# Kernel tuning notes

Measured on AMD Instinct MI355X. Metric: run time of the kernel, lower is better.

The kernel has to match this reference:

```python
import jax, jax.numpy as jnp
from jax import lax
import numpy as np

T, B, I, H, O = 512, 128, 256, 512, 256


def setup_inputs() -> dict:
    key = jax.random.key(0)
    ks = jax.random.split(key, 11)
    s = 0.05
    return {
        "x": jax.random.normal(ks[0], (T, B, I), dtype=jnp.float32),
        "W_ih0": jax.random.normal(ks[1], (H, I), dtype=jnp.float32) * s,
        "b_ih0": jax.random.normal(ks[2], (H,), dtype=jnp.float32) * s,
        "W_hh0": jax.random.normal(ks[3], (H, H), dtype=jnp.float32) * s,
        "b_hh0": jax.random.normal(ks[4], (H,), dtype=jnp.float32) * s,
        "W_ih1": jax.random.normal(ks[5], (H, H), dtype=jnp.float32) * s,
        "b_ih1": jax.random.normal(ks[6], (H,), dtype=jnp.float32) * s,
        "W_hh1": jax.random.normal(ks[7], (H, H), dtype=jnp.float32) * s,
        "b_hh1": jax.random.normal(ks[8], (H,), dtype=jnp.float32) * s,
        "W_fc": jax.random.normal(ks[9], (O, H), dtype=jnp.float32) * s,
        "b_fc": jax.random.normal(ks[10], (O,), dtype=jnp.float32) * s,
    }


def reference(x, W_ih0, b_ih0, W_hh0, b_hh0, W_ih1, b_ih1, W_hh1, b_hh1, W_fc, b_fc):
    # x: [T, B, I] (batch_first=False). 2-layer tanh RNN via lax.scan over time.
    Tn, Bn, _ = x.shape
    Hn = W_hh0.shape[0]
    h0 = jnp.zeros((2, Bn, Hn), dtype=x.dtype)

    def step(h, xt):
        h1 = jnp.tanh(xt @ W_ih0.T + b_ih0 + h[0] @ W_hh0.T + b_hh0)  # [B, H]
        h2 = jnp.tanh(h1 @ W_ih1.T + b_ih1 + h[1] @ W_hh1.T + b_hh1)  # [B, H]
        return jnp.stack([h1, h2]), h2

    h_final, out = lax.scan(step, h0, x)  # out: [T, B, H]
    # Faithful to source: output[:, -1, :] indexes the LAST BATCH element (batch_first=False),
    # giving [T, H]; pred is [T, O].
    pred = out[:, -1, :] @ W_fc.T + b_fc
    return pred, h_final
```

## Files before the change

kernel.cpp:

```cpp
#include <hip/hip_runtime.h>
#include <hip/hip_bf16.h>

#define TT 512
#define BB 128
#define II 256
#define HH 512
#define OO 256

#define NGB 8
#define NGN 16
#define RB  16
#define NS  32

#define PRED_SZ (TT*OO)

typedef __attribute__((ext_vector_type(8))) short bf16x8;
typedef __attribute__((ext_vector_type(4))) float f32x4;

#define WS_CNT  0
#define WS_H1   16512
#define WS_H2   (WS_H1 + 2*BB*HH*2)
#define WS_SAVE (WS_H2 + 2*BB*HH*2)
#define WS_ZERO WS_SAVE

__device__ __forceinline__ ushort f2bf(float f) {
  union { float f; unsigned u; } v; v.f = f;
  unsigned u = v.u;
  return (ushort)((u + 0x7FFFu + ((u >> 16) & 1u)) >> 16);
}

__global__ __launch_bounds__(256) void rnn_scan_kernel(
    const float* __restrict__ x,
    const float* __restrict__ Wih0, const float* __restrict__ bih0,
    const float* __restrict__ Whh0, const float* __restrict__ bhh0,
    const float* __restrict__ Wih1, const float* __restrict__ bih1,
    const float* __restrict__ Whh1, const float* __restrict__ bhh1,
    float* __restrict__ out, char* __restrict__ ws)
{
  __shared__ ushort ldsW[112*64*8];
  __shared__ float bias0[NS];
  __shared__ float bias1[NS];

  int*    cnt    = (int*)(ws + WS_CNT);
  ushort* h1buf  = (ushort*)(ws + WS_H1);
  ushort* h2buf  = (ushort*)(ws + WS_H2);
  float*  h2save = (float*)(ws + WS_SAVE);

  const int tid = threadIdx.x;
  const int gb  = blockIdx.x & 7;
  const int gn  = blockIdx.x >> 3;
  const int n0  = gn * NS;

  {
    const int lane = tid & 63;
    const int q    = tid >> 6;
    #pragma unroll 1
    for (int u = 0; u < 112; ++u) {
      const float* Wsrc; int Km; int ul;
      if (u < 16)      { Wsrc = Wih0; Km = II; ul = u; }
      else if (u < 48) { Wsrc = Whh0; Km = HH; ul = u - 16; }
      else if (u < 80) { Wsrc = Wih1; Km = HH; ul = u - 48; }
      else             { Wsrc = Whh1; Km = HH; ul = u - 80; }
      const int nk  = Km >> 5;
      const int ttl = ul / nk;
      const int kk  = ul - ttl*nk;
      const int n   = n0 + ttl*16 + (lane & 15);
      const int k   = kk*32 + (lane >> 4)*8 + q*2;
      const float2 wv = *(const float2*)(Wsrc + (size_t)n*Km + k);
      ushort2 b2; b2.x = f2bf(wv.x); b2.y = f2bf(wv.y);
      *(ushort2*)&ldsW[(u*64 + lane)*8 + q*2] = b2;
    }
    if (tid < NS) {
      bias0[tid] = bih0[n0+tid] + bhh0[n0+tid];
      bias1[tid] = bih1[n0+tid] + bhh1[n0+tid];
    }
  }
  __syncthreads();

  const int w     = tid >> 6;
  const int lane  = tid & 63;
  const int ttile = w & 1;
  const int layer = w >> 1;
  const int kq    = lane >> 4;
  const int rowg  = gb*RB + (lane & 15);
  const int c     = lane & 15;

  for (int p = 0; p <= TT; ++p) {
    f32x4 xf[16];
    if (layer == 0 && p < TT) {
      const float* xp = x + ((size_t)p*BB + rowg)*II + kq*8;
      #pragma unroll
      for (int kk = 0; kk < 8; ++kk) {
        xf[2*kk]   = *(const f32x4*)(xp + kk*32);
        xf[2*kk+1] = *(const f32x4*)(xp + kk*32 + 4);
      }
    }
    if (p > 0) {
      if (tid == 0) {
        while (__hip_atomic_load(&cnt[(p-1)*NGB + gb], __ATOMIC_ACQUIRE,
                                 __HIP_MEMORY_SCOPE_AGENT) < NGN) {
          __builtin_amdgcn_s_sleep(1);
        }
      }
      __syncthreads();
    }

    if (layer == 0) {
      if (p < TT) {
        bf16x8 af[16];
        const ushort* ap = h1buf + ((size_t)((p-1)&1)*BB + rowg)*HH + kq*8;
        #pragma unroll
        for (int kk = 0; kk < 16; ++kk) af[kk] = *(const bf16x8*)(ap + kk*32);
        f32x4 acc = {0.f,0.f,0.f,0.f};
        #pragma unroll
        for (int kk = 0; kk < 8; ++kk) {
          bf16x8 a;
          #pragma unroll
          for (int j = 0; j < 4; ++j) {
            a[j]   = (short)f2bf(xf[2*kk][j]);
            a[j+4] = (short)f2bf(xf[2*kk+1][j]);
          }
          const bf16x8 b = *(const bf16x8*)&ldsW[((0 + ttile*8 + kk)*64 + lane)*8];
          acc = __builtin_amdgcn_mfma_f32_16x16x32_bf16(a, b, acc, 0, 0, 0);
        }
        #pragma unroll
        for (int kk = 0; kk < 16; ++kk) {
          const bf16x8 b = *(const bf16x8*)&ldsW[((16 + ttile*16 + kk)*64 + lane)*8];
          acc = __builtin_amdgcn_mfma_f32_16x16x32_bf16(af[kk], b, acc, 0, 0, 0);
        }
        const float bv = bias0[ttile*16 + c];
        ushort* dst = h1buf + (size_t)(p&1)*BB*HH;
        const int col = n0 + ttile*16 + c;
        #pragma unroll
        for (int j = 0; j < 4; ++j) {
          const int r = gb*16 + kq*4 + j;
          const float v = tanhf(acc[j] + bv);
          dst[(size_t)r*HH + col] = f2bf(v);
          if (p == TT-1) out[PRED_SZ + (size_t)r*HH + col] = v;
        }
      }
    } else {
      if (p >= 1) {
        bf16x8 af[16], a2[16];
        const ushort* ap  = h1buf + ((size_t)((p-1)&1)*BB + rowg)*HH + kq*8;
        const ushort* a2p = h2buf + ((size_t)(p&1)*BB + rowg)*HH + kq*8;
        #pragma unroll
        for (int kk = 0; kk < 16; ++kk) {
          af[kk] = *(const bf16x8*)(ap  + kk*32);
          a2[kk] = *(const bf16x8*)(a2p + kk*32);
        }
        f32x4 acc = {0.f,0.f,0.f,0.f};
        #pragma unroll
        for (int kk = 0; kk < 16; ++kk) {
          const bf16x8 b = *(const bf16x8*)&ldsW[((48 + ttile*16 + kk)*64 + lane)*8];
          acc = __builtin_amdgcn_mfma_f32_16x16x32_bf16(af[kk], b, acc, 0, 0, 0);
        }
        #pragma unroll
        for (int kk = 0; kk < 16; ++kk) {
          const bf16x8 b = *(const bf16x8*)&ldsW[((80 + ttile*16 + kk)*64 + lane)*8];
          acc = __builtin_amdgcn_mfma_f32_16x16x32_bf16(a2[kk], b, acc, 0, 0, 0);
        }
        const float bv = bias1[ttile*16 + c];
        ushort* dst = h2buf + (size_t)((p-1)&1)*BB*HH;
        const int col = n0 + ttile*16 + c;
        #pragma unroll
        for (int j = 0; j < 4; ++j) {
          const int r = gb*16 + kq*4 + j;
          const float v = tanhf(acc[j] + bv);
          dst[(size_t)r*HH + col] = f2bf(v);
          if (r == BB-1) h2save[(size_t)(p-1)*HH + col] = v;
          if (p == TT) out[PRED_SZ + BB*HH + (size_t)r*HH + col] = v;
        }
      }
    }

    __syncthreads();
    if (tid == 0) {
      __hip_atomic_fetch_add(&cnt[p*NGB + gb], 1, __ATOMIC_RELEASE,
                             __HIP_MEMORY_SCOPE_AGENT);
    }
  }
}

__global__ __launch_bounds__(256) void rnn_pred_kernel(
    const float* __restrict__ Wfc, const float* __restrict__ bfc,
    const float* __restrict__ h2save, float* __restrict__ out)
{
  __shared__ float hs[HH];
  const int t = blockIdx.x;
  for (int i = threadIdx.x; i < HH; i += 256) hs[i] = h2save[(size_t)t*HH + i];
  __syncthreads();
  const int o = threadIdx.x;
  const f32x4* wr = (const f32x4*)(Wfc + (size_t)o*HH);
  f32x4 s = {0.f,0.f,0.f,0.f};
  #pragma unroll 8
  for (int k = 0; k < HH/4; ++k) {
    const f32x4 wv = wr[k];
    const f32x4 hv = *(const f32x4*)&hs[4*k];
    s += wv * hv;
  }
  out[(size_t)t*OO + o] = bfc[o] + s[0] + s[1] + s[2] + s[3];
}

extern "C" void kernel_launch(void* const* d_in, const int* in_sizes, int n_in,
                              void* d_out, int out_size, void* d_ws, size_t ws_size,
                              hipStream_t stream) {
  const float* x    = (const float*)d_in[0];
  const float* Wih0 = (const float*)d_in[1];
  const float* bih0 = (const float*)d_in[2];
  const float* Whh0 = (const float*)d_in[3];
  const float* bhh0 = (const float*)d_in[4];
  const float* Wih1 = (const float*)d_in[5];
  const float* bih1 = (const float*)d_in[6];
  const float* Whh1 = (const float*)d_in[7];
  const float* bhh1 = (const float*)d_in[8];
  const float* Wfc  = (const float*)d_in[9];
  const float* bfc  = (const float*)d_in[10];
  float* out = (float*)d_out;
  char*  ws  = (char*)d_ws;

  hipMemsetAsync(ws, 0, WS_ZERO, stream);

  rnn_scan_kernel<<<NGB*NGN, 256, 0, stream>>>(x, Wih0, bih0, Whh0, bhh0,
                                               Wih1, bih1, Whh1, bhh1, out, ws);
  rnn_pred_kernel<<<TT, 256, 0, stream>>>(Wfc, bfc, (const float*)(ws + WS_SAVE), out);
}
```

Baseline: 3.695 ms.

## Decouple RNN layers into per-wave pipelines with monotonic counters and coherent loads

Replaces the per-timestep block-wide barrier and per-step counter array with two monotonic per-batch-group counters, one per layer. Layer-0 and layer-1 waves now run independent loops and spin on the counters themselves, and layer 0 may run up to three steps ahead using a 4-deep h1 ring buffer. Cross-block h exchange uses cache-bypassing sc0 sc1 loads and stores with relaxed atomics instead of acquire/release. tanhf is replaced by an exp2/rcp approximation. Correctness now depends on the hand-written memory ordering through inline asm waitcnt, and the tanh is slightly less accurate.

```diff
diff --git a/kernel.cpp b/kernel.cpp
--- a/kernel.cpp
+++ b/kernel.cpp
@@ -16,10 +16,12 @@
 
 typedef __attribute__((ext_vector_type(8))) short bf16x8;
 typedef __attribute__((ext_vector_type(4))) float f32x4;
-
-#define WS_CNT  0
-#define WS_H1   16512
-#define WS_H2   (WS_H1 + 2*BB*HH*2)
+typedef __attribute__((ext_vector_type(4))) int   i32x4;
+
+#define WS_G1   0
+#define WS_G2   128
+#define WS_H1   256
+#define WS_H2   (WS_H1 + 4*BB*HH*2)
 #define WS_SAVE (WS_H2 + 2*BB*HH*2)
 #define WS_ZERO WS_SAVE
 
@@ -29,7 +31,32 @@
   return (ushort)((u + 0x7FFFu + ((u >> 16) & 1u)) >> 16);
 }
 
-__global__ __launch_bounds__(256) void rnn_scan_kernel(
+__device__ __forceinline__ float fast_tanh(float x) {
+  float cx = fminf(fmaxf(x, -30.f), 30.f);
+  float t  = __builtin_amdgcn_exp2f(cx * 2.885390081777927f);
+  return (t - 1.f) * __builtin_amdgcn_rcpf(t + 1.f);
+}
+
+__device__ __forceinline__ i32x4 ld_coh16B(const ushort* p) {
+  i32x4 r;
+  asm volatile("global_load_dwordx4 %0, %1, off sc0 sc1"
+               : "=v"(r) : "v"(p) : "memory");
+  return r;
+}
+__device__ __forceinline__ void st_coh2B(ushort* p, ushort v) {
+  unsigned vv = v;
+  asm volatile("global_store_short %0, %1, off sc0 sc1"
+               :: "v"(p), "v"(vv) : "memory");
+}
+
+__device__ __forceinline__ int g_load(int* a) {
+  return __hip_atomic_load(a, __ATOMIC_RELAXED, __HIP_MEMORY_SCOPE_AGENT);
+}
+__device__ __forceinline__ void g_post(int* a) {
+  __hip_atomic_fetch_add(a, 1, __ATOMIC_RELAXED, __HIP_MEMORY_SCOPE_AGENT);
+}
+
+__global__ __launch_bounds__(256, 1) void rnn_scan_kernel(
     const float* __restrict__ x,
     const float* __restrict__ Wih0, const float* __restrict__ bih0,
     const float* __restrict__ Whh0, const float* __restrict__ bhh0,
@@ -41,7 +68,8 @@
   __shared__ float bias0[NS];
   __shared__ float bias1[NS];
 
-  int*    cnt    = (int*)(ws + WS_CNT);
+  int*    g1     = (int*)(ws + WS_G1);
+  int*    g2     = (int*)(ws + WS_G2);
   ushort* h1buf  = (ushort*)(ws + WS_H1);
   ushort* h2buf  = (ushort*)(ws + WS_H2);
   float*  h2save = (float*)(ws + WS_SAVE);
@@ -85,99 +113,106 @@
   const int rowg  = gb*RB + (lane & 15);
   const int c     = lane & 15;
 
-  for (int p = 0; p <= TT; ++p) {
-    f32x4 xf[16];
-    if (layer == 0 && p < TT) {
-      const float* xp = x + ((size_t)p*BB + rowg)*II + kq*8;
-      #pragma unroll
-      for (int kk = 0; kk < 8; ++kk) {
-        xf[2*kk]   = *(const f32x4*)(xp + kk*32);
-        xf[2*kk+1] = *(const f32x4*)(xp + kk*32 + 4);
-      }
-    }
-    if (p > 0) {
-      if (tid == 0) {
-        while (__hip_atomic_load(&cnt[(p-1)*NGB + gb], __ATOMIC_ACQUIRE,
-                                 __HIP_MEMORY_SCOPE_AGENT) < NGN) {
-          __builtin_amdgcn_s_sleep(1);
+  int s1 = 0, s2 = 0;
+
+  if (layer == 0) {
+    for (int p = 0; p < TT; ++p) {
+      bf16x8 ax[8];
+      {
+        const float* xp = x + ((size_t)p*BB + rowg)*II + kq*8;
+        f32x4 xf[16];
+        #pragma unroll
+        for (int kk = 0; kk < 8; ++kk) {
+          xf[2*kk]   = *(const f32x4*)(xp + kk*32);
+          xf[2*kk+1] = *(const f32x4*)(xp + kk*32 + 4);
         }
-      }
-      __syncthreads();
-    }
-
-    if (layer == 0) {
-      if (p < TT) {
-        bf16x8 af[16];
-        const ushort* ap = h1buf + ((size_t)((p-1)&1)*BB + rowg)*HH + kq*8;
-        #pragma unroll
-        for (int kk = 0; kk < 16; ++kk) af[kk] = *(const bf16x8*)(ap + kk*32);
-        f32x4 acc = {0.f,0.f,0.f,0.f};
-        #pragma unroll
-        for (int kk = 0; kk < 8; ++kk) {
-          bf16x8 a;
+        #pragma unroll
+        for (int kk = 0; kk < 8; ++kk)
           #pragma unroll
           for (int j = 0; j < 4; ++j) {
-            a[j]   = (short)f2bf(xf[2*kk][j]);
-            a[j+4] = (short)f2bf(xf[2*kk+1][j]);
+            ax[kk][j]   = (short)f2bf(xf[2*kk][j]);
+            ax[kk][j+4] = (short)f2bf(xf[2*kk+1][j]);
           }
-          const bf16x8 b = *(const bf16x8*)&ldsW[((0 + ttile*8 + kk)*64 + lane)*8];
-          acc = __builtin_amdgcn_mfma_f32_16x16x32_bf16(a, b, acc, 0, 0, 0);
-        }
+      }
+      if (p >= 1 && s1 < 32*p)       { do { s1 = g_load(&g1[gb]); } while (s1 < 32*p); }
+      if (p >= 4 && s2 < 32*(p-3))   { do { s2 = g_load(&g2[gb]); } while (s2 < 32*(p-3)); }
+      asm volatile("" ::: "memory");
+
+      f32x4 acc = {0.f,0.f,0.f,0.f};
+      i32x4 af[16];
+      if (p >= 1) {
+        const ushort* ap = h1buf + ((size_t)((p-1)&3)*BB + rowg)*HH + kq*8;
+        #pragma unroll
+        for (int kk = 0; kk < 16; ++kk) af[kk] = ld_coh16B(ap + kk*32);
+      }
+      #pragma unroll
+      for (int kk = 0; kk < 8; ++kk) {
+        const bf16x8 b = *(const bf16x8*)&ldsW[((0 + ttile*8 + kk)*64 + lane)*8];
+        acc = __builtin_amdgcn_mfma_f32_16x16x32_bf16(ax[kk], b, acc, 0, 0, 0);
+      }
+      if (p >= 1) {
+        asm volatile("s_waitcnt vmcnt(0)" ::: "memory");
+        __builtin_amdgcn_sched_barrier(0);
         #pragma unroll
         for (int kk = 0; kk < 16; ++kk) {
           const bf16x8 b = *(const bf16x8*)&ldsW[((16 + ttile*16 + kk)*64 + lane)*8];
-          acc = __builtin_amdgcn_mfma_f32_16x16x32_bf16(af[kk], b, acc, 0, 0, 0);
+          acc = __builtin_amdgcn_mfma_f32_16x16x32_bf16(__builtin_bit_cast(bf16x8, af[kk]), b, acc, 0, 0, 0);
         }
-        const float bv = bias0[ttile*16 + c];
-        ushort* dst = h1buf + (size_t)(p&1)*BB*HH;
-        const int col = n0 + ttile*16 + c;
-        #pragma unroll
-        for (int j = 0; j < 4; ++j) {
-          const int r = gb*16 + kq*4 + j;
-          const float v = tanhf(acc[j] + bv);
-          dst[(size_t)r*HH + col] = f2bf(v);
-          if (p == TT-1) out[PRED_SZ + (size_t)r*HH + col] = v;
-        }
-      }
-    } else {
-      if (p >= 1) {
-        bf16x8 af[16], a2[16];
-        const ushort* ap  = h1buf + ((size_t)((p-1)&1)*BB + rowg)*HH + kq*8;
-        const ushort* a2p = h2buf + ((size_t)(p&1)*BB + rowg)*HH + kq*8;
-        #pragma unroll
-        for (int kk = 0; kk < 16; ++kk) {
-          af[kk] = *(const bf16x8*)(ap  + kk*32);
-          a2[kk] = *(const bf16x8*)(a2p + kk*32);
-        }
-        f32x4 acc = {0.f,0.f,0.f,0.f};
-        #pragma unroll
-        for (int kk = 0; kk < 16; ++kk) {
-          const bf16x8 b = *(const bf16x8*)&ldsW[((48 + ttile*16 + kk)*64 + lane)*8];
-          acc = __builtin_amdgcn_mfma_f32_16x16x32_bf16(af[kk], b, acc, 0, 0, 0);
-        }
-        #pragma unroll
-        for (int kk = 0; kk < 16; ++kk) {
-          const bf16x8 b = *(const bf16x8*)&ldsW[((80 + ttile*16 + kk)*64 + lane)*8];
-          acc = __builtin_amdgcn_mfma_f32_16x16x32_bf16(a2[kk], b, acc, 0, 0, 0);
-        }
-        const float bv = bias1[ttile*16 + c];
-        ushort* dst = h2buf + (size_t)((p-1)&1)*BB*HH;
-        const int col = n0 + ttile*16 + c;
-        #pragma unroll
-        for (int j = 0; j < 4; ++j) {
-          const int r = gb*16 + kq*4 + j;
-          const float v = tanhf(acc[j] + bv);
-          dst[(size_t)r*HH + col] = f2bf(v);
-          if (r == BB-1) h2save[(size_t)(p-1)*HH + col] = v;
-          if (p == TT) out[PRED_SZ + BB*HH + (size_t)r*HH + col] = v;
-        }
-      }
-    }
-
-    __syncthreads();
-    if (tid == 0) {
-      __hip_atomic_fetch_add(&cnt[p*NGB + gb], 1, __ATOMIC_RELEASE,
-                             __HIP_MEMORY_SCOPE_AGENT);
+      }
+      const float bv = bias0[ttile*16 + c];
+      ushort* dst = h1buf + (size_t)(p&3)*BB*HH;
+      const int col = n0 + ttile*16 + c;
+      #pragma unroll
+      for (int j = 0; j < 4; ++j) {
+        const int r = gb*16 + kq*4 + j;
+        const float v = fast_tanh(acc[j] + bv);
+        st_coh2B(dst + (size_t)r*HH + col, f2bf(v));
+        if (p == TT-1) out[PRED_SZ + (size_t)r*HH + col] = v;
+      }
+      asm volatile("s_waitcnt vmcnt(0)" ::: "memory");
+      if (lane == 0) g_post(&g1[gb]);
+    }
+  } else {
+    for (int p = 1; p <= TT; ++p) {
+      if (s1 < 32*p)                 { do { s1 = g_load(&g1[gb]); } while (s1 < 32*p); }
+      if (p >= 2 && s2 < 32*(p-1))   { do { s2 = g_load(&g2[gb]); } while (s2 < 32*(p-1)); }
+      asm volatile("" ::: "memory");
+
+      i32x4 af[16], a2[16];
+      const ushort* ap  = h1buf + ((size_t)((p-1)&3)*BB + rowg)*HH + kq*8;
+      const ushort* a2p = h2buf + ((size_t)(p&1)*BB + rowg)*HH + kq*8;
+      #pragma unroll
+      for (int kk = 0; kk < 16; ++kk) {
+        af[kk] = ld_coh16B(ap  + kk*32);
+        a2[kk] = ld_coh16B(a2p + kk*32);
+      }
+      asm volatile("s_waitcnt vmcnt(0)" ::: "memory");
+      __builtin_amdgcn_sched_barrier(0);
+
+      f32x4 acc = {0.f,0.f,0.f,0.f};
+      #pragma unroll
+      for (int kk = 0; kk < 16; ++kk) {
+        const bf16x8 b = *(const bf16x8*)&ldsW[((48 + ttile*16 + kk)*64 + lane)*8];
+        acc = __builtin_amdgcn_mfma_f32_16x16x32_bf16(__builtin_bit_cast(bf16x8, af[kk]), b, acc, 0, 0, 0);
+      }
+      #pragma unroll
+      for (int kk = 0; kk < 16; ++kk) {
+        const bf16x8 b = *(const bf16x8*)&ldsW[((80 + ttile*16 + kk)*64 + lane)*8];
+        acc = __builtin_amdgcn_mfma_f32_16x16x32_bf16(__builtin_bit_cast(bf16x8, a2[kk]), b, acc, 0, 0, 0);
+      }
+      const float bv = bias1[ttile*16 + c];
+      ushort* dst = h2buf + (size_t)((p-1)&1)*BB*HH;
+      const int col = n0 + ttile*16 + c;
+      #pragma unroll
+      for (int j = 0; j < 4; ++j) {
+        const int r = gb*16 + kq*4 + j;
+        const float v = fast_tanh(acc[j] + bv);
+        st_coh2B(dst + (size_t)r*HH + col, f2bf(v));
+        if (r == BB-1) h2save[(size_t)(p-1)*HH + col] = v;
+        if (p == TT) out[PRED_SZ + BB*HH + (size_t)r*HH + col] = v;
+      }
+      asm volatile("s_waitcnt vmcnt(0)" ::: "memory");
+      if (lane == 0) g_post(&g2[gb]);
     }
   }
 }
```

Result: slower. 5.158 ms (+39.6%).

## Split RNN scan by batch rows with per-layer blocks and register-resident weights

Applied to the files above, without the earlier changes.

Repartitions the persistent scan so each block owns four batch rows and one layer, holding the full weight matrices as bf16 MFMA fragments in registers. Hidden state then stays in LDS and global grid-wide barriers go away; layer 0 passes h1 to its paired layer-1 block through a ring buffer coordinated by flags. The change also adds a fast exp2/rcp tanh and cache-bypassing inline-asm loads and stores. It relies on co-residency of producer and consumer blocks and carries high register pressure at 1024 threads.

```diff
diff --git a/kernel.cpp b/kernel.cpp
--- a/kernel.cpp
+++ b/kernel.cpp
@@ -7,21 +7,25 @@
 #define HH 512
 #define OO 256
 
-#define NGB 8
-#define NGN 16
-#define RB  16
-#define NS  32
+#define PAIRS 32
+#define ROWS  4
+#define RING  8
+#define HP    520
+#define IP    264
 
 #define PRED_SZ (TT*OO)
 
 typedef __attribute__((ext_vector_type(8))) short bf16x8;
 typedef __attribute__((ext_vector_type(4))) float f32x4;
-
-#define WS_CNT  0
-#define WS_H1   16512
-#define WS_H2   (WS_H1 + 2*BB*HH*2)
-#define WS_SAVE (WS_H2 + 2*BB*HH*2)
-#define WS_ZERO WS_SAVE
+typedef __attribute__((ext_vector_type(4))) int   i32x4;
+typedef __attribute__((ext_vector_type(2))) int   i32x2;
+typedef __attribute__((ext_vector_type(2))) unsigned u32x2;
+
+#define WS_F1   0
+#define WS_F2   4096
+#define WS_RING 8192
+#define WS_SAVE (8192 + PAIRS*RING*ROWS*HH*2)
+#define WS_ZERO 8192
 
 __device__ __forceinline__ ushort f2bf(float f) {
   union { float f; unsigned u; } v; v.f = f;
@@ -29,7 +33,40 @@
   return (ushort)((u + 0x7FFFu + ((u >> 16) & 1u)) >> 16);
 }
 
-__global__ __launch_bounds__(256) void rnn_scan_kernel(
+__device__ __forceinline__ float fast_tanh(float x) {
+  float cx = fminf(fmaxf(x, -30.f), 30.f);
+  float t  = __builtin_amdgcn_exp2f(cx * 2.885390081777927f);
+  return (t - 1.f) * __builtin_amdgcn_rcpf(t + 1.f);
+}
+
+__device__ __forceinline__ i32x4 ld16(const ushort* p) {
+  i32x4 r;
+  asm volatile("global_load_dwordx4 %0, %1, off sc0 sc1" : "=v"(r) : "v"(p) : "memory");
+  return r;
+}
+__device__ __forceinline__ void st8(ushort* p, i32x2 v) {
+  asm volatile("global_store_dwordx2 %0, %1, off sc0 sc1" :: "v"(p), "v"(v) : "memory");
+}
+__device__ __forceinline__ void st_flag(int* p, int v) {
+  asm volatile("global_store_dword %0, %1, off sc0 sc1" :: "v"(p), "v"(v) : "memory");
+}
+__device__ __forceinline__ int ld_flag(const int* p) {
+  int r;
+  asm volatile("global_load_dword %0, %1, off sc0 sc1\n\ts_waitcnt vmcnt(0)"
+               : "=v"(r) : "v"(p) : "memory");
+  return r;
+}
+__device__ __forceinline__ void ldf_issue(const int* p, int& r) {
+  asm volatile("global_load_dword %0, %1, off sc0 sc1" : "=v"(r) : "v"(p) : "memory");
+}
+#define WAIT_VM(N) asm volatile("s_waitcnt vmcnt(" #N ")" ::: "memory")
+#define SBAR() __builtin_amdgcn_sched_barrier(0)
+
+__device__ __forceinline__ f32x4 MFMA(bf16x8 a, bf16x8 b, f32x4 c) {
+  return __builtin_amdgcn_mfma_f32_16x16x32_bf16(a, b, c, 0, 0, 0);
+}
+
+__global__ __launch_bounds__(1024) void rnn_scan_kernel(
     const float* __restrict__ x,
     const float* __restrict__ Wih0, const float* __restrict__ bih0,
     const float* __restrict__ Whh0, const float* __restrict__ bhh0,
@@ -37,147 +74,237 @@
     const float* __restrict__ Whh1, const float* __restrict__ bhh1,
     float* __restrict__ out, char* __restrict__ ws)
 {
-  __shared__ ushort ldsW[112*64*8];
-  __shared__ float bias0[NS];
-  __shared__ float bias1[NS];
-
-  int*    cnt    = (int*)(ws + WS_CNT);
-  ushort* h1buf  = (ushort*)(ws + WS_H1);
-  ushort* h2buf  = (ushort*)(ws + WS_H2);
+  __shared__ ushort bufA[2][ROWS][HP];
+  __shared__ ushort bufB[2][ROWS][HP];
+  __shared__ ushort xst[2][ROWS][IP];
+  __shared__ int arr;
+
+  int*    flag1  = (int*)(ws + WS_F1);
+  int*    flag2  = (int*)(ws + WS_F2);
+  ushort* ring   = (ushort*)(ws + WS_RING);
   float*  h2save = (float*)(ws + WS_SAVE);
 
-  const int tid = threadIdx.x;
-  const int gb  = blockIdx.x & 7;
-  const int gn  = blockIdx.x >> 3;
-  const int n0  = gn * NS;
+  const int  bid  = blockIdx.x;
+  const int  pair = bid & (PAIRS-1);
+  const bool isL1 = bid >= PAIRS;
+  const int  tid  = threadIdx.x;
+  const int  w    = tid >> 6;
+  const int  lane = tid & 63;
+  const int  kq   = lane >> 4;
+  const int  c    = lane & 15;
+  const int  rl   = c & 3;
+  const int  cb0  = 32*w;
+  const int  cw   = kq*4;
+  ushort* ringp = ring + (size_t)pair*RING*ROWS*HH;
+  int* f1p = flag1 + pair*32;
+  int* f2p = flag2 + pair*32;
 
   {
-    const int lane = tid & 63;
-    const int q    = tid >> 6;
-    #pragma unroll 1
-    for (int u = 0; u < 112; ++u) {
-      const float* Wsrc; int Km; int ul;
-      if (u < 16)      { Wsrc = Wih0; Km = II; ul = u; }
-      else if (u < 48) { Wsrc = Whh0; Km = HH; ul = u - 16; }
-      else if (u < 80) { Wsrc = Wih1; Km = HH; ul = u - 48; }
-      else             { Wsrc = Whh1; Km = HH; ul = u - 80; }
-      const int nk  = Km >> 5;
-      const int ttl = ul / nk;
-      const int kk  = ul - ttl*nk;
-      const int n   = n0 + ttl*16 + (lane & 15);
-      const int k   = kk*32 + (lane >> 4)*8 + q*2;
-      const float2 wv = *(const float2*)(Wsrc + (size_t)n*Km + k);
-      ushort2 b2; b2.x = f2bf(wv.x); b2.y = f2bf(wv.y);
-      *(ushort2*)&ldsW[(u*64 + lane)*8 + q*2] = b2;
-    }
-    if (tid < NS) {
-      bias0[tid] = bih0[n0+tid] + bhh0[n0+tid];
-      bias1[tid] = bih1[n0+tid] + bhh1[n0+tid];
-    }
+    ushort* zA = &bufA[1][0][0];
+    ushort* zB = &bufB[1][0][0];
+    for (int i = tid; i < ROWS*HP; i += 1024) { zA[i] = 0; zB[i] = 0; }
+    if (tid == 0) arr = 0;
   }
-  __syncthreads();
-
-  const int w     = tid >> 6;
-  const int lane  = tid & 63;
-  const int ttile = w & 1;
-  const int layer = w >> 1;
-  const int kq    = lane >> 4;
-  const int rowg  = gb*RB + (lane & 15);
-  const int c     = lane & 15;
-
-  for (int p = 0; p <= TT; ++p) {
-    f32x4 xf[16];
-    if (layer == 0 && p < TT) {
-      const float* xp = x + ((size_t)p*BB + rowg)*II + kq*8;
-      #pragma unroll
-      for (int kk = 0; kk < 8; ++kk) {
-        xf[2*kk]   = *(const f32x4*)(xp + kk*32);
-        xf[2*kk+1] = *(const f32x4*)(xp + kk*32 + 4);
-      }
-    }
-    if (p > 0) {
-      if (tid == 0) {
-        while (__hip_atomic_load(&cnt[(p-1)*NGB + gb], __ATOMIC_ACQUIRE,
-                                 __HIP_MEMORY_SCOPE_AGENT) < NGN) {
-          __builtin_amdgcn_s_sleep(1);
+
+  auto ldfrag = [&](const float* W, int ldk, int n, int k) -> bf16x8 {
+    const float* p = W + (size_t)n*ldk + k;
+    const f32x4 v0 = *(const f32x4*)p;
+    const f32x4 v1 = *(const f32x4*)(p+4);
+    bf16x8 r;
+    #pragma unroll
+    for (int j = 0; j < 4; ++j) { r[j] = (short)f2bf(v0[j]); r[j+4] = (short)f2bf(v1[j]); }
+    return r;
+  };
+
+  if (!isL1) {
+    bf16x8 whh[2][16], wih[2][8];
+    f32x4 bias[2];
+    #pragma unroll
+    for (int t = 0; t < 2; ++t) {
+      #pragma unroll
+      for (int kk = 0; kk < 16; ++kk) whh[t][kk] = ldfrag(Whh0, HH, cb0 + 16*t + c, 32*kk + kq*8);
+      #pragma unroll
+      for (int kk = 0; kk < 8;  ++kk) wih[t][kk] = ldfrag(Wih0, II, cb0 + 16*t + c, 32*kk + kq*8);
+      const int nb = cb0 + 16*t + cw;
+      bias[t] = (f32x4){ bih0[nb]+bhh0[nb], bih0[nb+1]+bhh0[nb+1],
+                         bih0[nb+2]+bhh0[nb+2], bih0[nb+3]+bhh0[nb+3] };
+    }
+    if (w == 14) {
+      const float* xp = x + (size_t)pair*ROWS*II;
+      #pragma unroll
+      for (int i = 0; i < 4; ++i) {
+        const f32x4 v = *(const f32x4*)(xp + i*256 + lane*4);
+        u32x2 d;
+        d.x = (unsigned)f2bf(v[0]) | ((unsigned)f2bf(v[1]) << 16);
+        d.y = (unsigned)f2bf(v[2]) | ((unsigned)f2bf(v[3]) << 16);
+        *(u32x2*)&xst[0][i][lane*4] = d;
+      }
+    }
+    __syncthreads();
+
+    int vf2 = 0;
+    for (int p = 0; p < TT; ++p) {
+      int f2v = vf2;
+      if (p >= RING) ldf_issue(f2p, f2v);
+      f32x4 xv[4];
+      const bool stgx = (w == 14 && p+1 < TT);
+      if (stgx) {
+        const float* xp = x + ((size_t)(p+1)*BB + pair*ROWS)*II;
+        #pragma unroll
+        for (int i = 0; i < 4; ++i) xv[i] = *(const f32x4*)(xp + i*256 + lane*4);
+      }
+      f32x4 a0 = {0.f,0.f,0.f,0.f}, a1 = {0.f,0.f,0.f,0.f};
+      {
+        const ushort* hb = &bufA[(p-1)&1][rl][0];
+        #pragma unroll
+        for (int kk = 0; kk < 16; ++kk) {
+          const bf16x8 hf = *(const bf16x8*)&hb[32*kk + kq*8];
+          a0 = MFMA(whh[0][kk], hf, a0);
+          a1 = MFMA(whh[1][kk], hf, a1);
+        }
+        const ushort* xb = &xst[p&1][rl][0];
+        #pragma unroll
+        for (int kk = 0; kk < 8; ++kk) {
+          const bf16x8 xf = *(const bf16x8*)&xb[32*kk + kq*8];
+          a0 = MFMA(wih[0][kk], xf, a0);
+          a1 = MFMA(wih[1][kk], xf, a1);
+        }
+      }
+      f32x4 o0, o1;
+      #pragma unroll
+      for (int j = 0; j < 4; ++j) {
+        o0[j] = fast_tanh(a0[j] + bias[0][j]);
+        o1[j] = fast_tanh(a1[j] + bias[1][j]);
+      }
+      WAIT_VM(0); SBAR();
+      if (lane == 0 && p >= 1) {
+        int old = atomicAdd(&arr, 1);
+        if (old == 16*p - 1) st_flag(f1p, p);
+      }
+      if (p >= RING) {
+        if (!__all(f2v >= p - RING)) {
+          do { f2v = ld_flag(f2p); } while (!__all(f2v >= p - RING));
+        }
+        vf2 = f2v;
+      }
+      u32x2 d0, d1;
+      d0.x = (unsigned)f2bf(o0[0]) | ((unsigned)f2bf(o0[1]) << 16);
+      d0.y = (unsigned)f2bf(o0[2]) | ((unsigned)f2bf(o0[3]) << 16);
+      d1.x = (unsigned)f2bf(o1[0]) | ((unsigned)f2bf(o1[1]) << 16);
+      d1.y = (unsigned)f2bf(o1[2]) | ((unsigned)f2bf(o1[3]) << 16);
+      if (c < ROWS) {
+        *(u32x2*)&bufA[p&1][c][cb0 + cw]      = d0;
+        *(u32x2*)&bufA[p&1][c][cb0 + 16 + cw] = d1;
+        ushort* rp = ringp + ((size_t)(p&(RING-1))*ROWS + c)*HH + cb0 + cw;
+        st8(rp,      (i32x2){(int)d0.x, (int)d0.y});
+        st8(rp + 16, (i32x2){(int)d1.x, (int)d1.y});
+        if (p == TT-1) {
+          float* op = out + PRED_SZ + (size_t)(pair*ROWS + c)*HH + cb0 + cw;
+          *(f32x4*)op        = o0;
+          *(f32x4*)(op + 16) = o1;
+        }
+      }
+      if (stgx) {
+        #pragma unroll
+        for (int i = 0; i < 4; ++i) {
+          u32x2 d;
+          d.x = (unsigned)f2bf(xv[i][0]) | ((unsigned)f2bf(xv[i][1]) << 16);
+          d.y = (unsigned)f2bf(xv[i][2]) | ((unsigned)f2bf(xv[i][3]) << 16);
+          *(u32x2*)&xst[(p+1)&1][i][lane*4] = d;
         }
       }
       __syncthreads();
     }
-
-    if (layer == 0) {
-      if (p < TT) {
-        bf16x8 af[16];
-        const ushort* ap = h1buf + ((size_t)((p-1)&1)*BB + rowg)*HH + kq*8;
-        #pragma unroll
-        for (int kk = 0; kk < 16; ++kk) af[kk] = *(const bf16x8*)(ap + kk*32);
-        f32x4 acc = {0.f,0.f,0.f,0.f};
-        #pragma unroll
-        for (int kk = 0; kk < 8; ++kk) {
-          bf16x8 a;
-          #pragma unroll
-          for (int j = 0; j < 4; ++j) {
-            a[j]   = (short)f2bf(xf[2*kk][j]);
-            a[j+4] = (short)f2bf(xf[2*kk+1][j]);
-          }
-          const bf16x8 b = *(const bf16x8*)&ldsW[((0 + ttile*8 + kk)*64 + lane)*8];
-          acc = __builtin_amdgcn_mfma_f32_16x16x32_bf16(a, b, acc, 0, 0, 0);
-        }
+    WAIT_VM(0);
+    if (lane == 0) {
+      int old = atomicAdd(&arr, 1);
+      if (old == 16*TT - 1) st_flag(f1p, TT);
+    }
+  } else {
+    bf16x8 wih[2][16], whh[2][16];
+    f32x4 bias[2];
+    #pragma unroll
+    for (int t = 0; t < 2; ++t) {
+      #pragma unroll
+      for (int kk = 0; kk < 16; ++kk) {
+        wih[t][kk] = ldfrag(Wih1, HH, cb0 + 16*t + c, 32*kk + kq*8);
+        whh[t][kk] = ldfrag(Whh1, HH, cb0 + 16*t + c, 32*kk + kq*8);
+      }
+      const int nb = cb0 + 16*t + cw;
+      bias[t] = (f32x4){ bih1[nb]+bhh1[nb], bih1[nb+1]+bhh1[nb+1],
+                         bih1[nb+2]+bhh1[nb+2], bih1[nb+3]+bhh1[nb+3] };
+    }
+    __syncthreads();
+
+    int f1v = 0;
+    if (w == 15) {
+      do { f1v = ld_flag(f1p); } while (f1v < 1);
+      const ushort* rp = ringp + lane*8;
+      i32x4 rv[4];
+      #pragma unroll
+      for (int i = 0; i < 4; ++i) rv[i] = ld16(rp + i*HH);
+      WAIT_VM(0); SBAR();
+      #pragma unroll
+      for (int i = 0; i < 4; ++i) *(i32x4*)&bufA[0][i][lane*8] = rv[i];
+      st_flag(f2p, 0);
+    }
+    __syncthreads();
+
+    for (int p = 1; p <= TT; ++p) {
+      i32x4 rv[4];
+      const bool stg = (w == 15 && p < TT);
+      if (stg) {
+        if (f1v < p+1) { do { f1v = ld_flag(f1p); } while (f1v < p+1); }
+        const ushort* rp = ringp + (size_t)(p&(RING-1))*ROWS*HH + lane*8;
+        #pragma unroll
+        for (int i = 0; i < 4; ++i) rv[i] = ld16(rp + i*HH);
+      }
+      f32x4 a0 = {0.f,0.f,0.f,0.f}, a1 = {0.f,0.f,0.f,0.f};
+      {
+        const ushort* h1b = &bufA[(p-1)&1][rl][0];
+        const ushort* h2b = &bufB[p&1][rl][0];
         #pragma unroll
         for (int kk = 0; kk < 16; ++kk) {
-          const bf16x8 b = *(const bf16x8*)&ldsW[((16 + ttile*16 + kk)*64 + lane)*8];
-          acc = __builtin_amdgcn_mfma_f32_16x16x32_bf16(af[kk], b, acc, 0, 0, 0);
-        }
-        const float bv = bias0[ttile*16 + c];
-        ushort* dst = h1buf + (size_t)(p&1)*BB*HH;
-        const int col = n0 + ttile*16 + c;
-        #pragma unroll
-        for (int j = 0; j < 4; ++j) {
-          const int r = gb*16 + kq*4 + j;
-          const float v = tanhf(acc[j] + bv);
-          dst[(size_t)r*HH + col] = f2bf(v);
-          if (p == TT-1) out[PRED_SZ + (size_t)r*HH + col] = v;
-        }
-      }
-    } else {
-      if (p >= 1) {
-        bf16x8 af[16], a2[16];
-        const ushort* ap  = h1buf + ((size_t)((p-1)&1)*BB + rowg)*HH + kq*8;
-        const ushort* a2p = h2buf + ((size_t)(p&1)*BB + rowg)*HH + kq*8;
-        #pragma unroll
-        for (int kk = 0; kk < 16; ++kk) {
-          af[kk] = *(const bf16x8*)(ap  + kk*32);
-          a2[kk] = *(const bf16x8*)(a2p + kk*32);
-        }
-        f32x4 acc = {0.f,0.f,0.f,0.f};
-        #pragma unroll
-        for (int kk = 0; kk < 16; ++kk) {
-          const bf16x8 b = *(const bf16x8*)&ldsW[((48 + ttile*16 + kk)*64 + lane)*8];
-          acc = __builtin_amdgcn_mfma_f32_16x16x32_bf16(af[kk], b, acc, 0, 0, 0);
-        }
-        #pragma unroll
-        for (int kk = 0; kk < 16; ++kk) {
-          const bf16x8 b = *(const bf16x8*)&ldsW[((80 + ttile*16 + kk)*64 + lane)*8];
-          acc = __builtin_amdgcn_mfma_f32_16x16x32_bf16(a2[kk], b, acc, 0, 0, 0);
-        }
-        const float bv = bias1[ttile*16 + c];
-        ushort* dst = h2buf + (size_t)((p-1)&1)*BB*HH;
-        const int col = n0 + ttile*16 + c;
-        #pragma unroll
-        for (int j = 0; j < 4; ++j) {
-          const int r = gb*16 + kq*4 + j;
-          const float v = tanhf(acc[j] + bv);
-          dst[(size_t)r*HH + col] = f2bf(v);
-          if (r == BB-1) h2save[(size_t)(p-1)*HH + col] = v;
-          if (p == TT) out[PRED_SZ + BB*HH + (size_t)r*HH + col] = v;
-        }
-      }
-    }
-
-    __syncthreads();
-    if (tid == 0) {
-      __hip_atomic_fetch_add(&cnt[p*NGB + gb], 1, __ATOMIC_RELEASE,
-                             __HIP_MEMORY_SCOPE_AGENT);
+          const bf16x8 f1f = *(const bf16x8*)&h1b[32*kk + kq*8];
+          const bf16x8 f2f = *(const bf16x8*)&h2b[32*kk + kq*8];
+          a0 = MFMA(wih[0][kk], f1f, a0);
+          a1 = MFMA(wih[1][kk], f1f, a1);
+          a0 = MFMA(whh[0][kk], f2f, a0);
+          a1 = MFMA(whh[1][kk], f2f, a1);
+        }
+      }
+      f32x4 o0, o1;
+      #pragma unroll
+      for (int j = 0; j < 4; ++j) {
+        o0[j] = fast_tanh(a0[j] + bias[0][j]);
+        o1[j] = fast_tanh(a1[j] + bias[1][j]);
+      }
+      if (stg) {
+        WAIT_VM(0); SBAR();
+        #pragma unroll
+        for (int i = 0; i < 4; ++i) *(i32x4*)&bufA[p&1][i][lane*8] = rv[i];
+        st_flag(f2p, p);
+      }
+      if (c < ROWS) {
+        u32x2 d0, d1;
+        d0.x = (unsigned)f2bf(o0[0]) | ((unsigned)f2bf(o0[1]) << 16);
+        d0.y = (unsigned)f2bf(o0[2]) | ((unsigned)f2bf(o0[3]) << 16);
+        d1.x = (unsigned)f2bf(o1[0]) | ((unsigned)f2bf(o1[1]) << 16);
+        d1.y = (unsigned)f2bf(o1[2]) | ((unsigned)f2bf(o1[3]) << 16);
+        *(u32x2*)&bufB[(p-1)&1][c][cb0 + cw]      = d0;
+        *(u32x2*)&bufB[(p-1)&1][c][cb0 + 16 + cw] = d1;
+        if (pair == PAIRS-1 && c == ROWS-1) {
+          float* sp = h2save + (size_t)(p-1)*HH + cb0 + cw;
+          *(f32x4*)sp        = o0;
+          *(f32x4*)(sp + 16) = o1;
+        }
+        if (p == TT) {
+          float* op = out + PRED_SZ + BB*HH + (size_t)(pair*ROWS + c)*HH + cb0 + cw;
+          *(f32x4*)op        = o0;
+          *(f32x4*)(op + 16) = o1;
+        }
+      }
+      __syncthreads();
     }
   }
 }
@@ -221,7 +348,7 @@
 
   hipMemsetAsync(ws, 0, WS_ZERO, stream);
 
-  rnn_scan_kernel<<<NGB*NGN, 256, 0, stream>>>(x, Wih0, bih0, Whh0, bhh0,
-                                               Wih1, bih1, Whh1, bhh1, out, ws);
+  rnn_scan_kernel<<<2*PAIRS, 1024, 0, stream>>>(x, Wih0, bih0, Whh0, bhh0,
+                                                Wih1, bih1, Whh1, bhh1, out, ws);
   rnn_pred_kernel<<<TT, 256, 0, stream>>>(Wfc, bfc, (const float*)(ws + WS_SAVE), out);
 }
```

After: 11.63 ms. 3.15x slower.
